# Kernel tuning notes

Measured on AMD Instinct MI355X. Metric: run time of the kernel, lower is better.

## Reference

```python
import jax, jax.numpy as jnp
import numpy as np

EPS = 1e-6

def _ln(x, w, b):
    mu = jnp.mean(x, axis=-1, keepdims=True)
    var = jnp.mean((x - mu) ** 2, axis=-1, keepdims=True)
    return (x - mu) * jax.lax.rsqrt(var + EPS) * w + b

def setup_inputs() -> dict:
    B, N, C, H, P = 64, 197, 768, 12, 20
    Dh = C // H
    Dff = 4 * C
    key = jax.random.key(0)
    ks = jax.random.split(key, 16)
    s = 0.02
    return {
        "x": jax.random.normal(ks[0], (B, N, C), jnp.float32),
        "prompt": jax.random.normal(ks[1], (B, P, 2, H, Dh), jnp.float32),
        "ln1_w": jnp.ones((C,), jnp.float32),
        "ln1_b": jnp.zeros((C,), jnp.float32),
        "qkv_w": jax.random.normal(ks[2], (3 * C, C), jnp.float32) * s,
        "qkv_b": jnp.zeros((3 * C,), jnp.float32),
        "proj_w": jax.random.normal(ks[3], (C, C), jnp.float32) * s,
        "proj_b": jnp.zeros((C,), jnp.float32),
        "ln2_w": jnp.ones((C,), jnp.float32),
        "ln2_b": jnp.zeros((C,), jnp.float32),
        "fc1_w": jax.random.normal(ks[4], (Dff, C), jnp.float32) * s,
        "fc1_b": jnp.zeros((Dff,), jnp.float32),
        "fc2_w": jax.random.normal(ks[5], (C, Dff), jnp.float32) * s,
        "fc2_b": jnp.zeros((C,), jnp.float32),
    }

def reference(x, prompt, ln1_w, ln1_b, qkv_w, qkv_b, proj_w, proj_b,
              ln2_w, ln2_b, fc1_w, fc1_b, fc2_w, fc2_b):
    B, N, C = x.shape
    H = 12
    Dh = C // H
    scale = Dh ** -0.5

    # --- attention branch ---
    h = _ln(x, ln1_w, ln1_b)
    qkv = (h @ qkv_w.T + qkv_b).reshape(B, N, 3, H, Dh)
    qkv = jnp.transpose(qkv, (2, 0, 3, 1, 4))  # [3, B, H, N, Dh]
    q, k, v = qkv[0], qkv[1], qkv[2]

    # prompt: [B, P, 2, H, Dh] -> [2, B, H, P, Dh]
    pr = jnp.transpose(prompt, (2, 0, 3, 1, 4))
    k = jnp.concatenate([pr[0], k], axis=2)  # [B, H, P+N, Dh]
    v = jnp.concatenate([pr[1], v], axis=2)

    attn = jnp.einsum('bhnd,bhmd->bhnm', q, k) * scale
    attn = jax.nn.softmax(attn, axis=-1)
    o = jnp.einsum('bhnm,bhmd->bhnd', attn, v)
    o = jnp.transpose(o, (0, 2, 1, 3)).reshape(B, N, C)
    o = o @ proj_w.T + proj_b
    x = x + o

    # --- mlp branch ---
    h2 = _ln(x, ln2_w, ln2_b)
    m = jax.nn.gelu(h2 @ fc1_w.T + fc1_b, approximate=False)
    m = m @ fc2_w.T + fc2_b
    return x + m
```

## Files before the change

kernel.cpp:

```cpp
#include <hip/hip_runtime.h>
#include <hip/hip_bf16.h>

typedef __attribute__((ext_vector_type(4))) float f32x4;
typedef __attribute__((ext_vector_type(8))) __bf16 bfv8;
typedef __attribute__((ext_vector_type(8))) short sv8;
typedef __attribute__((ext_vector_type(4))) unsigned short usv4;


static __device__ __forceinline__ f32x4 mfma16(sv8 a, sv8 b, f32x4 c) {
    return __builtin_amdgcn_mfma_f32_16x16x32_bf16(
        __builtin_bit_cast(bfv8, a), __builtin_bit_cast(bfv8, b), c, 0, 0, 0);
}

static __device__ __forceinline__ unsigned short f2bf(float f) {
    union { float f; unsigned int u; } v; v.f = f;
    unsigned int u = v.u;
    return (unsigned short)((u + 0x7FFFu + ((u >> 16) & 1u)) >> 16);
}

static __device__ __forceinline__ void gld16(void* lds, const void* g) {
    __builtin_amdgcn_global_load_lds(
        (const __attribute__((address_space(1))) unsigned int*)g,
        (__attribute__((address_space(3))) unsigned int*)lds, 16, 0, 0);
}


__global__ void cvt_bf16_kernel(const float* __restrict__ in,
                                unsigned short* __restrict__ out, int n4) {
    int i = blockIdx.x * 256 + threadIdx.x;
    if (i >= n4) return;
    float4 f = reinterpret_cast<const float4*>(in)[i];
    usv4 o = { f2bf(f.x), f2bf(f.y), f2bf(f.z), f2bf(f.w) };
    reinterpret_cast<usv4*>(out)[i] = o;
}


__global__ void ln_kernel(const float* __restrict__ x, const float* __restrict__ w,
                          const float* __restrict__ b, unsigned short* __restrict__ out) {
    const int row = blockIdx.x;
    const int t = threadIdx.x;
    const float* xr = x + (size_t)row * 768;
    float v[3];
    float s = 0.f, ss = 0.f;
#pragma unroll
    for (int i = 0; i < 3; ++i) {
        v[i] = xr[t + i * 256];
        s += v[i]; ss += v[i] * v[i];
    }
#pragma unroll
    for (int o = 32; o; o >>= 1) { s += __shfl_xor(s, o); ss += __shfl_xor(ss, o); }
    __shared__ float red[8];
    if ((t & 63) == 0) { red[t >> 6] = s; red[4 + (t >> 6)] = ss; }
    __syncthreads();
    float S = red[0] + red[1] + red[2] + red[3];
    float SS = red[4] + red[5] + red[6] + red[7];
    float mu = S * (1.0f / 768.0f);
    float var = SS * (1.0f / 768.0f) - mu * mu;
    float rstd = rsqrtf(var + 1e-6f);
#pragma unroll
    for (int i = 0; i < 3; ++i) {
        int c = t + i * 256;
        out[(size_t)row * 768 + c] = f2bf((v[i] - mu) * rstd * w[c] + b[c]);
    }
}


__global__ void prompt_kernel(const float* __restrict__ pr,
                              unsigned short* __restrict__ k_out,
                              unsigned short* __restrict__ v_out) {
    int i = blockIdx.x * 256 + threadIdx.x;
    if (i >= 64 * 20 * 12 * 64) return;
    int d = i & 63;
    int t = i >> 6;
    int h = t % 12;
    int t2 = t / 12;
    int p = t2 % 20;
    int b = t2 / 20;
    size_t src = ((((size_t)b * 20 + p) * 2 + 0) * 12 + h) * 64 + d;
    float kv = pr[src];
    float vv = pr[src + 12 * 64];
    k_out[(((size_t)(b * 12 + h) * 224 + p) << 6) + d] = f2bf(kv);
    v_out[((size_t)(b * 12 + h) * 64 + d) * 224 + p] = f2bf(vv);
}


#define EPI_QKV 0
#define EPI_RES 1
#define EPI_GELU 2

template <int EPI, int WM, int WN>
__global__ void __launch_bounds__(WM * WN * 64)
gemm_bf16(const unsigned short* __restrict__ A,
          const unsigned short* __restrict__ W,
          const float* __restrict__ bias,
          const float* __restrict__ resid,
          void* __restrict__ out0,
          unsigned short* __restrict__ q_out,
          unsigned short* __restrict__ k_out,
          unsigned short* __restrict__ v_out,
          int M, int N, int K, int NB) {
    constexpr int THREADS = WM * WN * 64;
    constexpr int BM = WM * 64, BN = WN * 64;
    constexpr int NCA = (BM * 4) / THREADS;
    constexpr int NCB = (BN * 4) / THREADS;
    __shared__ __align__(16) unsigned short As[2][BM * 32];
    __shared__ __align__(16) unsigned short Bs[2][BN * 32];
    const int tid = threadIdx.x;
    const int lane = tid & 63;
    const int wv = tid >> 6;
    const int wm = wv / WN, wn = wv % WN;
    const int rl = lane & 15, kg = lane >> 4;

    const int nwg = gridDim.x;
    const int orig = blockIdx.x;
    const int xcd = orig & 7;
    const int qq = nwg >> 3, rr = nwg & 7;
    const int wg = (xcd < rr ? xcd * (qq + 1) : rr * (qq + 1) + (xcd - rr) * qq) + (orig >> 3);
    const int bm = wg / NB, bn = wg - bm * NB;

    const unsigned short* pA[NCA];
    const unsigned short* pB[NCB];
#pragma unroll
    for (int i = 0; i < NCA; ++i) {
        const int c = i * THREADS + tid;
        const int row = c >> 2, sl = c & 3;
        int ar = bm * BM + row; ar = ar < M ? ar : M - 1;
        pA[i] = A + (size_t)ar * K + sl * 8;
    }
#pragma unroll
    for (int i = 0; i < NCB; ++i) {
        const int c = i * THREADS + tid;
        const int row = c >> 2, sl = c & 3;
        pB[i] = W + (size_t)(bn * BN + row) * K + sl * 8;
    }
    auto stage = [&](int sb, int kt) {
        const int k0 = kt << 5;
#pragma unroll
        for (int i = 0; i < NCA; ++i)
            gld16(&As[sb][(i * THREADS + tid) * 8], pA[i] + k0);
#pragma unroll
        for (int i = 0; i < NCB; ++i)
            gld16(&Bs[sb][(i * THREADS + tid) * 8], pB[i] + k0);
    };

    f32x4 acc[4][4];
#pragma unroll
    for (int i = 0; i < 4; ++i)
#pragma unroll
        for (int j = 0; j < 4; ++j) acc[i][j] = f32x4{0.f, 0.f, 0.f, 0.f};

    const int nk = K >> 5;
    stage(0, 0);
    __syncthreads();
    for (int kt = 0; kt < nk; ++kt) {
        const int cur = kt & 1;
        if (kt + 1 < nk) stage(cur ^ 1, kt + 1);
        sv8 af[4], bfr[4];
#pragma unroll
        for (int f = 0; f < 4; ++f) {
            const int ra = wm * 64 + f * 16 + rl;
            af[f] = *reinterpret_cast<const sv8*>(&As[cur][ra * 32 + kg * 8]);
            const int rb = wn * 64 + f * 16 + rl;
            bfr[f] = *reinterpret_cast<const sv8*>(&Bs[cur][rb * 32 + kg * 8]);
        }
#pragma unroll
        for (int i = 0; i < 4; ++i)
#pragma unroll
            for (int j = 0; j < 4; ++j) acc[i][j] = mfma16(af[i], bfr[j], acc[i][j]);
        __syncthreads();
    }

#pragma unroll
    for (int i = 0; i < 4; ++i) {
        const int m0 = bm * BM + wm * 64 + i * 16 + kg * 4;
#pragma unroll
        for (int j = 0; j < 4; ++j) {
            const int ncol = bn * BN + wn * 64 + j * 16 + rl;
            const float bia = bias[ncol];
#pragma unroll
            for (int r = 0; r < 4; ++r) {
                const int m = m0 + r;
                if (m >= M) continue;
                float vv = acc[i][j][r] + bia;
                if constexpr (EPI == EPI_QKV) {
                    int b = m / 197, nn = m - b * 197;
                    int which = ncol / 768;
                    int rc = ncol - which * 768;
                    int h = rc >> 6;
                    int d = ncol & 63;
                    if (which == 0)
                        q_out[(((size_t)(b * 12 + h) * 197 + nn) << 6) + d] = f2bf(vv);
                    else if (which == 1)
                        k_out[(((size_t)(b * 12 + h) * 224 + 20 + nn) << 6) + d] = f2bf(vv);
                    else
                        v_out[((size_t)(b * 12 + h) * 64 + d) * 224 + 20 + nn] = f2bf(vv);
                } else if constexpr (EPI == EPI_RES) {
                    ((float*)out0)[(size_t)m * N + ncol] = vv + resid[(size_t)m * N + ncol];
                } else {
                    float g = vv / (1.0f + __expf(-1.5957691216f * vv * (1.0f + 0.044715f * vv * vv)));
                    ((unsigned short*)out0)[(size_t)m * N + ncol] = f2bf(g);
                }
            }
        }
    }
}


__global__ void attn_kernel(const unsigned short* __restrict__ Qg,
                            const unsigned short* __restrict__ Kg,
                            const unsigned short* __restrict__ Vtg,
                            unsigned short* __restrict__ obuf) {
    __shared__ __align__(16) unsigned short sKS[14848];
    __shared__ __align__(16) unsigned short sV[64 * 232];
    const int tid = threadIdx.x;
    const int lane = tid & 63;
    const int wave = tid >> 6;
    const int rl = lane & 15, kg = lane >> 4;
    const int qt = blockIdx.x, h = blockIdx.y, b = blockIdx.z;
    const size_t bh = (size_t)b * 12 + h;
    const size_t qbase = bh * 197 * 64;
    const size_t kbase = bh * 224 * 64;
    const size_t vbase = bh * 64 * 224;

    int qrow = qt * 64 + wave * 16 + rl;
    if (qrow > 196) qrow = 196;
    sv8 qf[2];
#pragma unroll
    for (int ks = 0; ks < 2; ++ks)
        qf[ks] = *reinterpret_cast<const sv8*>(&Qg[qbase + (size_t)qrow * 64 + ks * 32 + kg * 8]);

#pragma unroll
    for (int i = 0; i < 7; ++i) {
        const int c = i * 256 + tid;
        const int key = c >> 3, sl = c & 7;
        const int ssl = sl ^ (key & 7);
        gld16(&sKS[c * 8], &Kg[kbase + key * 64 + ssl * 8]);
    }
#pragma unroll
    for (int i = 0; i < 7; ++i) {
        const int c = i * 256 + tid;
        const int d = c / 28, sl = c - d * 28;
        sv8 val = *reinterpret_cast<const sv8*>(&Vtg[vbase + d * 224 + sl * 8]);
        *reinterpret_cast<sv8*>(&sV[d * 232 + sl * 8]) = val;
    }
    __syncthreads();

    f32x4 sacc[14];
#pragma unroll
    for (int f = 0; f < 14; ++f) sacc[f] = f32x4{0.f, 0.f, 0.f, 0.f};
#pragma unroll
    for (int f = 0; f < 14; ++f) {
        const int key = f * 16 + rl;
#pragma unroll
        for (int ks = 0; ks < 2; ++ks) {
            const int sl = (ks * 4 + kg) ^ (key & 7);
            sv8 kf = *reinterpret_cast<const sv8*>(&sKS[key * 64 + sl * 8]);
            sacc[f] = mfma16(qf[ks], kf, sacc[f]);
        }
    }

    float mx[4] = {-1e30f, -1e30f, -1e30f, -1e30f};
#pragma unroll
    for (int f = 0; f < 14; ++f) {
        const int col = f * 16 + rl;
#pragma unroll
        for (int r = 0; r < 4; ++r) {
            float s = sacc[f][r] * 0.125f;
            if (col >= 217) s = -1e30f;
            sacc[f][r] = s;
            mx[r] = fmaxf(mx[r], s);
        }
    }
#pragma unroll
    for (int o = 1; o < 16; o <<= 1)
#pragma unroll
        for (int r = 0; r < 4; ++r) mx[r] = fmaxf(mx[r], __shfl_xor(mx[r], o));
    float sm[4] = {0.f, 0.f, 0.f, 0.f};
#pragma unroll
    for (int f = 0; f < 14; ++f)
#pragma unroll
        for (int r = 0; r < 4; ++r) {
            float e = __expf(sacc[f][r] - mx[r]);
            sacc[f][r] = e;
            sm[r] += e;
        }
#pragma unroll
    for (int o = 1; o < 16; o <<= 1)
#pragma unroll
        for (int r = 0; r < 4; ++r) sm[r] += __shfl_xor(sm[r], o);
    float inv[4];
#pragma unroll
    for (int r = 0; r < 4; ++r) inv[r] = 1.0f / sm[r];

    __syncthreads();
    unsigned short* Sl = sKS;
#pragma unroll
    for (int f = 0; f < 14; ++f)
#pragma unroll
        for (int r = 0; r < 4; ++r)
            Sl[(wave * 16 + kg * 4 + r) * 232 + f * 16 + rl] = f2bf(sacc[f][r] * inv[r]);
    __syncthreads();

    f32x4 oacc[4];
#pragma unroll
    for (int fd = 0; fd < 4; ++fd) oacc[fd] = f32x4{0.f, 0.f, 0.f, 0.f};
#pragma unroll
    for (int ks = 0; ks < 7; ++ks) {
        sv8 pf = *reinterpret_cast<const sv8*>(&Sl[(wave * 16 + rl) * 232 + ks * 32 + kg * 8]);
#pragma unroll
        for (int fd = 0; fd < 4; ++fd) {
            sv8 vf = *reinterpret_cast<const sv8*>(&sV[(fd * 16 + rl) * 232 + ks * 32 + kg * 8]);
            oacc[fd] = mfma16(pf, vf, oacc[fd]);
        }
    }

#pragma unroll
    for (int fd = 0; fd < 4; ++fd)
#pragma unroll
        for (int r = 0; r < 4; ++r) {
            const int q = qt * 64 + wave * 16 + kg * 4 + r;
            if (q < 197)
                obuf[((size_t)b * 197 + q) * 768 + h * 64 + fd * 16 + rl] = f2bf(oacc[fd][r]);
        }
}


extern "C" void kernel_launch(void* const* d_in, const int* in_sizes, int n_in,
                              void* d_out, int out_size, void* d_ws, size_t ws_size,
                              hipStream_t stream) {
    const float* x      = (const float*)d_in[0];
    const float* prompt = (const float*)d_in[1];
    const float* ln1_w  = (const float*)d_in[2];
    const float* ln1_b  = (const float*)d_in[3];
    const float* qkv_w  = (const float*)d_in[4];
    const float* qkv_b  = (const float*)d_in[5];
    const float* proj_w = (const float*)d_in[6];
    const float* proj_b = (const float*)d_in[7];
    const float* ln2_w  = (const float*)d_in[8];
    const float* ln2_b  = (const float*)d_in[9];
    const float* fc1_w  = (const float*)d_in[10];
    const float* fc1_b  = (const float*)d_in[11];
    const float* fc2_w  = (const float*)d_in[12];
    const float* fc2_b  = (const float*)d_in[13];

    char* ws = (char*)d_ws;
    size_t off = 0;
    auto bump = [&](size_t bytes) {
        char* p = ws + off;
        off += (bytes + 255) & ~(size_t)255;
        return p;
    };
    unsigned short* qkvw  = (unsigned short*)bump(2304UL * 768 * 2);
    unsigned short* projw = (unsigned short*)bump(768UL * 768 * 2);
    unsigned short* fc1w  = (unsigned short*)bump(3072UL * 768 * 2);
    unsigned short* fc2w  = (unsigned short*)bump(768UL * 3072 * 2);
    unsigned short* h2    = (unsigned short*)bump(12608UL * 768 * 2);
    float* xmid           = (float*)bump(12608UL * 768 * 4);
    char* pool = ws + off;
    unsigned short* h1   = (unsigned short*)(pool);
    unsigned short* Qg   = (unsigned short*)(pool + 19365888UL);
    unsigned short* Kg   = (unsigned short*)(pool + 38731776UL);
    unsigned short* Vtg  = (unsigned short*)(pool + 60751872UL);
    unsigned short* obuf = (unsigned short*)(pool + 82771968UL);
    unsigned short* mbuf = (unsigned short*)(pool);

    cvt_bf16_kernel<<<(2304 * 768 / 4 + 255) / 256, 256, 0, stream>>>(qkv_w, qkvw, 2304 * 768 / 4);
    cvt_bf16_kernel<<<(768 * 768 / 4 + 255) / 256, 256, 0, stream>>>(proj_w, projw, 768 * 768 / 4);
    cvt_bf16_kernel<<<(3072 * 768 / 4 + 255) / 256, 256, 0, stream>>>(fc1_w, fc1w, 3072 * 768 / 4);
    cvt_bf16_kernel<<<(768 * 3072 / 4 + 255) / 256, 256, 0, stream>>>(fc2_w, fc2w, 768 * 3072 / 4);

    ln_kernel<<<12608, 256, 0, stream>>>(x, ln1_w, ln1_b, h1);
    prompt_kernel<<<983040 / 256, 256, 0, stream>>>(prompt, Kg, Vtg);

    gemm_bf16<EPI_QKV, 4, 4><<<50 * 9, 1024, 0, stream>>>(
        h1, qkvw, qkv_b, nullptr, nullptr, Qg, Kg, Vtg, 12608, 2304, 768, 9);

    attn_kernel<<<dim3(4, 12, 64), 256, 0, stream>>>(Qg, Kg, Vtg, obuf);

    gemm_bf16<EPI_RES, 2, 2><<<99 * 6, 256, 0, stream>>>(
        obuf, projw, proj_b, x, xmid, nullptr, nullptr, nullptr, 12608, 768, 768, 6);

    ln_kernel<<<12608, 256, 0, stream>>>(xmid, ln2_w, ln2_b, h2);

    gemm_bf16<EPI_GELU, 4, 4><<<50 * 12, 1024, 0, stream>>>(
        h2, fc1w, fc1_b, nullptr, mbuf, nullptr, nullptr, nullptr, 12608, 3072, 768, 12);

    gemm_bf16<EPI_RES, 2, 2><<<99 * 6, 256, 0, stream>>>(
        mbuf, fc2w, fc2_b, xmid, (float*)d_out, nullptr, nullptr, nullptr, 12608, 768, 3072, 6);
}
```

Baseline: 444.2 us.

## Add wave-private barrier-free GEMM for MLP and retile QKV GEMM

Adds a new GEMM kernel in which each wave stages its own 64-row A and B slices into private LDS buffers. It synchronises with s_waitcnt counters instead of __syncthreads and keeps two loads in flight. FC1 and FC2 now use this kernel with 128x128 block tiles, and the QKV GEMM moves from 256x256 to 256x128 tiles with 512 threads. The goal is to remove block-wide barrier stalls and improve occupancy, at the cost of loading A and B redundantly per wave, since waves sharing rows or columns no longer share LDS tiles.

```diff
diff --git a/kernel.cpp b/kernel.cpp
--- a/kernel.cpp
+++ b/kernel.cpp
@@ -83,99 +83,23 @@
     v_out[((size_t)(b * 12 + h) * 64 + d) * 224 + p] = f2bf(vv);
 }
 
-
 #define EPI_QKV 0
 #define EPI_RES 1
 #define EPI_GELU 2
 
-template <int EPI, int WM, int WN>
-__global__ void __launch_bounds__(WM * WN * 64)
-gemm_bf16(const unsigned short* __restrict__ A,
-          const unsigned short* __restrict__ W,
-          const float* __restrict__ bias,
-          const float* __restrict__ resid,
-          void* __restrict__ out0,
-          unsigned short* __restrict__ q_out,
-          unsigned short* __restrict__ k_out,
-          unsigned short* __restrict__ v_out,
-          int M, int N, int K, int NB) {
-    constexpr int THREADS = WM * WN * 64;
-    constexpr int BM = WM * 64, BN = WN * 64;
-    constexpr int NCA = (BM * 4) / THREADS;
-    constexpr int NCB = (BN * 4) / THREADS;
-    __shared__ __align__(16) unsigned short As[2][BM * 32];
-    __shared__ __align__(16) unsigned short Bs[2][BN * 32];
-    const int tid = threadIdx.x;
-    const int lane = tid & 63;
-    const int wv = tid >> 6;
-    const int wm = wv / WN, wn = wv % WN;
-    const int rl = lane & 15, kg = lane >> 4;
-
-    const int nwg = gridDim.x;
-    const int orig = blockIdx.x;
-    const int xcd = orig & 7;
-    const int qq = nwg >> 3, rr = nwg & 7;
-    const int wg = (xcd < rr ? xcd * (qq + 1) : rr * (qq + 1) + (xcd - rr) * qq) + (orig >> 3);
-    const int bm = wg / NB, bn = wg - bm * NB;
-
-    const unsigned short* pA[NCA];
-    const unsigned short* pB[NCB];
-#pragma unroll
-    for (int i = 0; i < NCA; ++i) {
-        const int c = i * THREADS + tid;
-        const int row = c >> 2, sl = c & 3;
-        int ar = bm * BM + row; ar = ar < M ? ar : M - 1;
-        pA[i] = A + (size_t)ar * K + sl * 8;
-    }
-#pragma unroll
-    for (int i = 0; i < NCB; ++i) {
-        const int c = i * THREADS + tid;
-        const int row = c >> 2, sl = c & 3;
-        pB[i] = W + (size_t)(bn * BN + row) * K + sl * 8;
-    }
-    auto stage = [&](int sb, int kt) {
-        const int k0 = kt << 5;
-#pragma unroll
-        for (int i = 0; i < NCA; ++i)
-            gld16(&As[sb][(i * THREADS + tid) * 8], pA[i] + k0);
-#pragma unroll
-        for (int i = 0; i < NCB; ++i)
-            gld16(&Bs[sb][(i * THREADS + tid) * 8], pB[i] + k0);
-    };
-
-    f32x4 acc[4][4];
-#pragma unroll
-    for (int i = 0; i < 4; ++i)
-#pragma unroll
-        for (int j = 0; j < 4; ++j) acc[i][j] = f32x4{0.f, 0.f, 0.f, 0.f};
-
-    const int nk = K >> 5;
-    stage(0, 0);
-    __syncthreads();
-    for (int kt = 0; kt < nk; ++kt) {
-        const int cur = kt & 1;
-        if (kt + 1 < nk) stage(cur ^ 1, kt + 1);
-        sv8 af[4], bfr[4];
-#pragma unroll
-        for (int f = 0; f < 4; ++f) {
-            const int ra = wm * 64 + f * 16 + rl;
-            af[f] = *reinterpret_cast<const sv8*>(&As[cur][ra * 32 + kg * 8]);
-            const int rb = wn * 64 + f * 16 + rl;
-            bfr[f] = *reinterpret_cast<const sv8*>(&Bs[cur][rb * 32 + kg * 8]);
-        }
-#pragma unroll
-        for (int i = 0; i < 4; ++i)
-#pragma unroll
-            for (int j = 0; j < 4; ++j) acc[i][j] = mfma16(af[i], bfr[j], acc[i][j]);
-        __syncthreads();
-    }
-
+
+template <int EPI>
+static __device__ __forceinline__ void gemm_epilogue(
+        f32x4 (&acc)[4][4], int bmBase, int bnBase, int wm, int wn,
+        int rl, int kg, const float* bias, const float* resid, void* out0,
+        unsigned short* q_out, unsigned short* k_out, unsigned short* v_out,
+        int M, int N) {
 #pragma unroll
     for (int i = 0; i < 4; ++i) {
-        const int m0 = bm * BM + wm * 64 + i * 16 + kg * 4;
+        const int m0 = bmBase + wm * 64 + i * 16 + kg * 4;
 #pragma unroll
         for (int j = 0; j < 4; ++j) {
-            const int ncol = bn * BN + wn * 64 + j * 16 + rl;
+            const int ncol = bnBase + wn * 64 + j * 16 + rl;
             const float bia = bias[ncol];
 #pragma unroll
             for (int r = 0; r < 4; ++r) {
@@ -206,6 +130,174 @@
 }
 
 
+template <int EPI, int WM, int WN>
+__global__ void __launch_bounds__(WM * WN * 64)
+gemm_bf16(const unsigned short* __restrict__ A,
+          const unsigned short* __restrict__ W,
+          const float* __restrict__ bias,
+          const float* __restrict__ resid,
+          void* __restrict__ out0,
+          unsigned short* __restrict__ q_out,
+          unsigned short* __restrict__ k_out,
+          unsigned short* __restrict__ v_out,
+          int M, int N, int K, int NB) {
+    constexpr int THREADS = WM * WN * 64;
+    constexpr int BM = WM * 64, BN = WN * 64;
+    constexpr int NCA = (BM * 4) / THREADS;
+    constexpr int NCB = (BN * 4) / THREADS;
+    __shared__ __align__(16) unsigned short As[2][BM * 32];
+    __shared__ __align__(16) unsigned short Bs[2][BN * 32];
+    const int tid = threadIdx.x;
+    const int lane = tid & 63;
+    const int wv = tid >> 6;
+    const int wm = wv / WN, wn = wv % WN;
+    const int rl = lane & 15, kg = lane >> 4;
+
+    const int nwg = gridDim.x;
+    const int orig = blockIdx.x;
+    const int xcd = orig & 7;
+    const int qq = nwg >> 3, rr = nwg & 7;
+    const int wg = (xcd < rr ? xcd * (qq + 1) : rr * (qq + 1) + (xcd - rr) * qq) + (orig >> 3);
+    const int bm = wg / NB, bn = wg - bm * NB;
+
+    const unsigned short* pA[NCA];
+    const unsigned short* pB[NCB];
+#pragma unroll
+    for (int i = 0; i < NCA; ++i) {
+        const int c = i * THREADS + tid;
+        const int row = c >> 2, sl = c & 3;
+        int ar = bm * BM + row; ar = ar < M ? ar : M - 1;
+        pA[i] = A + (size_t)ar * K + sl * 8;
+    }
+#pragma unroll
+    for (int i = 0; i < NCB; ++i) {
+        const int c = i * THREADS + tid;
+        const int row = c >> 2, sl = c & 3;
+        pB[i] = W + (size_t)(bn * BN + row) * K + sl * 8;
+    }
+    auto stage = [&](int sb, int kt) {
+        const int k0 = kt << 5;
+#pragma unroll
+        for (int i = 0; i < NCA; ++i)
+            gld16(&As[sb][(i * THREADS + tid) * 8], pA[i] + k0);
+#pragma unroll
+        for (int i = 0; i < NCB; ++i)
+            gld16(&Bs[sb][(i * THREADS + tid) * 8], pB[i] + k0);
+    };
+
+    f32x4 acc[4][4];
+#pragma unroll
+    for (int i = 0; i < 4; ++i)
+#pragma unroll
+        for (int j = 0; j < 4; ++j) acc[i][j] = f32x4{0.f, 0.f, 0.f, 0.f};
+
+    const int nk = K >> 5;
+    stage(0, 0);
+    __syncthreads();
+    for (int kt = 0; kt < nk; ++kt) {
+        const int cur = kt & 1;
+        if (kt + 1 < nk) stage(cur ^ 1, kt + 1);
+        sv8 af[4], bfr[4];
+#pragma unroll
+        for (int f = 0; f < 4; ++f) {
+            const int ra = wm * 64 + f * 16 + rl;
+            af[f] = *reinterpret_cast<const sv8*>(&As[cur][ra * 32 + kg * 8]);
+            const int rb = wn * 64 + f * 16 + rl;
+            bfr[f] = *reinterpret_cast<const sv8*>(&Bs[cur][rb * 32 + kg * 8]);
+        }
+#pragma unroll
+        for (int i = 0; i < 4; ++i)
+#pragma unroll
+            for (int j = 0; j < 4; ++j) acc[i][j] = mfma16(af[i], bfr[j], acc[i][j]);
+        __syncthreads();
+    }
+    gemm_epilogue<EPI>(acc, bm * BM, bn * BN, wm, wn, rl, kg, bias, resid,
+                       out0, q_out, k_out, v_out, M, N);
+}
+
+
+template <int EPI>
+__global__ void __launch_bounds__(256)
+gemm_wp(const unsigned short* __restrict__ A,
+        const unsigned short* __restrict__ W,
+        const float* __restrict__ bias,
+        const float* __restrict__ resid,
+        void* __restrict__ out0,
+        int M, int N, int K, int NB) {
+    __shared__ __align__(16) unsigned short L[2][4][4096];
+    const int tid = threadIdx.x;
+    const int lane = tid & 63;
+    const int wave = tid >> 6;
+    const int wm = wave >> 1, wn = wave & 1;
+    const int rl = lane & 15, kg = lane >> 4;
+
+    const int nwg = gridDim.x;
+    const int orig = blockIdx.x;
+    const int xcd = orig & 7;
+    const int qq = nwg >> 3, rr = nwg & 7;
+    const int wg = (xcd < rr ? xcd * (qq + 1) : rr * (qq + 1) + (xcd - rr) * qq) + (orig >> 3);
+    const int bm = wg / NB, bn = wg - bm * NB;
+
+    const unsigned short* gA[4];
+    const unsigned short* gB[4];
+#pragma unroll
+    for (int i = 0; i < 4; ++i) {
+        const int c = i * 64 + lane;
+        const int row = c >> 2, sl = c & 3;
+        int ar = bm * 128 + wm * 64 + row; ar = ar < M ? ar : M - 1;
+        gA[i] = A + (size_t)ar * K + sl * 8;
+        gB[i] = W + (size_t)(bn * 128 + wn * 64 + row) * K + sl * 8;
+    }
+    unsigned short* myL0 = &L[0][wave][0];
+    unsigned short* myL1 = &L[1][wave][0];
+
+    auto stage = [&](int sb, int kt) {
+        unsigned short* base = sb ? myL1 : myL0;
+        const int k0 = kt << 5;
+#pragma unroll
+        for (int i = 0; i < 4; ++i) {
+            const int c8 = (i * 64 + lane) * 8;
+            gld16(base + c8, gA[i] + k0);
+            gld16(base + 2048 + c8, gB[i] + k0);
+        }
+    };
+
+    f32x4 acc[4][4];
+#pragma unroll
+    for (int i = 0; i < 4; ++i)
+#pragma unroll
+        for (int j = 0; j < 4; ++j) acc[i][j] = f32x4{0.f, 0.f, 0.f, 0.f};
+
+    const int nk = K >> 5;
+    stage(0, 0);
+    stage(1, 1);
+    for (int kt = 0; kt < nk; ++kt) {
+        const int cur = kt & 1;
+        if (kt + 1 < nk)
+            asm volatile("s_waitcnt vmcnt(8)" ::: "memory");
+        else
+            asm volatile("s_waitcnt vmcnt(0)" ::: "memory");
+        const unsigned short* base = cur ? myL1 : myL0;
+        sv8 af[4], bfr[4];
+#pragma unroll
+        for (int f = 0; f < 4; ++f) {
+            af[f]  = *reinterpret_cast<const sv8*>(base + (f * 16 + rl) * 32 + kg * 8);
+            bfr[f] = *reinterpret_cast<const sv8*>(base + 2048 + (f * 16 + rl) * 32 + kg * 8);
+        }
+        if (kt + 2 < nk) {
+            asm volatile("s_waitcnt lgkmcnt(0)" ::: "memory");
+            stage(cur, kt + 2);
+        }
+#pragma unroll
+        for (int i = 0; i < 4; ++i)
+#pragma unroll
+            for (int j = 0; j < 4; ++j) acc[i][j] = mfma16(af[i], bfr[j], acc[i][j]);
+    }
+    gemm_epilogue<EPI>(acc, bm * 128, bn * 128, wm, wn, rl, kg, bias, resid,
+                       out0, nullptr, nullptr, nullptr, M, N);
+}
+
+
 __global__ void attn_kernel(const unsigned short* __restrict__ Qg,
                             const unsigned short* __restrict__ Kg,
                             const unsigned short* __restrict__ Vtg,
@@ -372,8 +464,8 @@
     ln_kernel<<<12608, 256, 0, stream>>>(x, ln1_w, ln1_b, h1);
     prompt_kernel<<<983040 / 256, 256, 0, stream>>>(prompt, Kg, Vtg);
 
-    gemm_bf16<EPI_QKV, 4, 4><<<50 * 9, 1024, 0, stream>>>(
-        h1, qkvw, qkv_b, nullptr, nullptr, Qg, Kg, Vtg, 12608, 2304, 768, 9);
+    gemm_bf16<EPI_QKV, 4, 2><<<50 * 18, 512, 0, stream>>>(
+        h1, qkvw, qkv_b, nullptr, nullptr, Qg, Kg, Vtg, 12608, 2304, 768, 18);
 
     attn_kernel<<<dim3(4, 12, 64), 256, 0, stream>>>(Qg, Kg, Vtg, obuf);
 
@@ -382,9 +474,9 @@
 
     ln_kernel<<<12608, 256, 0, stream>>>(xmid, ln2_w, ln2_b, h2);
 
-    gemm_bf16<EPI_GELU, 4, 4><<<50 * 12, 1024, 0, stream>>>(
-        h2, fc1w, fc1_b, nullptr, mbuf, nullptr, nullptr, nullptr, 12608, 3072, 768, 12);
-
-    gemm_bf16<EPI_RES, 2, 2><<<99 * 6, 256, 0, stream>>>(
-        mbuf, fc2w, fc2_b, xmid, (float*)d_out, nullptr, nullptr, nullptr, 12608, 768, 3072, 6);
-}
+    gemm_wp<EPI_GELU><<<99 * 24, 256, 0, stream>>>(
+        h2, fc1w, fc1_b, nullptr, mbuf, 12608, 3072, 768, 24);
+
+    gemm_wp<EPI_RES><<<99 * 6, 256, 0, stream>>>(
+        mbuf, fc2w, fc2_b, xmid, (float*)d_out, 12608, 768, 3072, 6);
+}
```

Measured after the change: 537.0 us. 1.21x slower.
